# Optimization experiments

Measured on AMD Instinct MI355X. Metric: run time of the kernel, lower is better.

## Reference

```python
import jax, jax.numpy as jnp
import numpy as np

# ---- DMP constants (DMPParameters(N=5, tau=1, dt=1/(T*l), Dof=1)) ----
N = 5
T = 10
L_SUB = 10
DT = 1.0 / (T * L_SUB)          # 0.01
A_X = 1.0
A_Z = 25.0
B_Z = A_Z / 4.0
TIME_STEPS = T * L_SUB + 1       # 101
_C = jnp.exp(-A_X * jnp.linspace(0.0, 1.0, N)).astype(jnp.float32)        # RBF centers
_SIGMA2 = ((N ** 1.5) / _C / A_X).astype(jnp.float32)                     # RBF widths


def _conv1d(x, w, b, pad):
    # x: [B, Cin, L], w: [Cout, Cin, K]
    y = jax.lax.conv_general_dilated(x, w, window_strides=(1,), padding=[(pad, pad)],
                                     dimension_numbers=("NCH", "OIH", "NCH"))
    return y + b[None, :, None]


def _forward(input, y0, conv1_w, conv1_b, conv2_w, conv2_b, fc_w, fc_b, L_w, L_b):
    B = input.shape[0]
    # ---- TSFEEGNet (CNN feature extractor) -> [B, 404] ----
    h = jax.nn.relu(_conv1d(input, conv1_w, conv1_b, 3))     # [B, 64, 384]
    h = h.reshape(B, h.shape[1], -1, 4).mean(-1)             # avgpool4 -> [B, 64, 96]
    h = jax.nn.relu(_conv1d(h, conv2_w, conv2_b, 2))         # [B, 128, 96]
    h = h.reshape(B, h.shape[1], -1, 4).mean(-1)             # [B, 128, 24]
    feat = h.reshape(B, -1)                                  # [B, 3072]
    output = feat @ fc_w.T + fc_b                            # [B, 404]
    # ---- s = L(output): per-sample time scaling tau ----
    s = output @ L_w.T + L_b                                 # [B, 1]
    tau = s[:, 0]                                            # [B]
    # ---- DMPIntegrator.forward (Dof=1): goal=output[:,0], w=output[:,1:6] ----
    goal = output[:, 0]                                      # [B]
    w = output[:, 1:1 + N]                                   # [B, N]
    y0v = y0.reshape(-1)                                     # [B]
    dy0 = jnp.zeros_like(y0v) + 0.01

    def step(carry, _):
        x, y, z = carry
        x = x + (-A_X * x * tau * DT)                        # canonical system
        psi = jnp.exp(-0.5 * (x[:, None] - _C[None, :]) ** 2 / _SIGMA2[None, :])  # [B, N]
        fx = (w * psi).sum(-1) * x * (goal - y0v) / psi.sum(-1)
        dz = A_Z * (B_Z * (goal - y) - z) + fx
        dy = z
        y = y + dy * tau * DT
        z = z + dz * tau * DT
        return (x, y, z), y

    x0 = jnp.ones_like(y0v)
    z0 = dy0 * tau
    _, Ys = jax.lax.scan(step, (x0, y0v, z0), None, length=TIME_STEPS - 1)  # [T-1, B]
    Y = jnp.concatenate([y0v[None, :], Ys], axis=0)          # [T, B]
    y_traj = Y.T.reshape(B, 1, TIME_STEPS)                   # [B, Dof=1, T]
    return y_traj.transpose(0, 2, 1)                         # [B, T, 1]


def setup_inputs():
    key = jax.random.key(0)
    ks = jax.random.split(key, 10)
    B = 4096
    sc = 0.05
    return {
        "input": jax.random.normal(ks[0], (B, 5, 384), jnp.float32),
        "y0": jax.random.normal(ks[1], (B,), jnp.float32),
        "conv1_w": jax.random.normal(ks[2], (64, 5, 7), jnp.float32) * sc,
        "conv1_b": jax.random.normal(ks[3], (64,), jnp.float32) * sc,
        "conv2_w": jax.random.normal(ks[4], (128, 64, 5), jnp.float32) * sc,
        "conv2_b": jax.random.normal(ks[5], (128,), jnp.float32) * sc,
        "fc_w": jax.random.normal(ks[6], (404, 3072), jnp.float32) * sc,
        "fc_b": jax.random.normal(ks[7], (404,), jnp.float32) * sc,
        "L_w": jax.random.normal(ks[8], (1, 404), jnp.float32) * sc,
        "L_b": jax.random.normal(ks[9], (1,), jnp.float32) * sc,
    }


def reference(input, y0, conv1_w, conv1_b, conv2_w, conv2_b, fc_w, fc_b, L_w, L_b):
    return _forward(input, y0, conv1_w, conv1_b, conv2_w, conv2_b, fc_w, fc_b, L_w, L_b)
```

## Files before the change

kernel.cpp:

```cpp
#include <hip/hip_runtime.h>
#include <math.h>


typedef short bf16x8 __attribute__((ext_vector_type(8)));
typedef _Float16 f16x8 __attribute__((ext_vector_type(8)));
typedef float f32x4  __attribute__((ext_vector_type(4)));
typedef float f32x16 __attribute__((ext_vector_type(16)));
typedef int   i32x4  __attribute__((ext_vector_type(4)));

union Frag { int u[4]; i32x4 q; bf16x8 v; f16x8 h; };
union H16 { _Float16 hf; unsigned short us; };

__device__ __forceinline__ unsigned short f16_rne(float f) {
    H16 c; c.hf = (_Float16)f; return c.us;
}

#define ZERO16 {0.f,0.f,0.f,0.f,0.f,0.f,0.f,0.f,0.f,0.f,0.f,0.f,0.f,0.f,0.f,0.f}

__global__ void precompute_kernel(const float* __restrict__ w1,
                                  const float* __restrict__ w2,
                                  const float* __restrict__ fc_w,
                                  const float* __restrict__ fc_b,
                                  const float* __restrict__ L_w,
                                  const float* __restrict__ L_b,
                                  float* __restrict__ fc7,
                                  float* __restrict__ taub,
                                  unsigned* __restrict__ wfrag1,
                                  unsigned* __restrict__ wfrag2) {
    const int t = threadIdx.x, bb = blockIdx.x;
    if (bb < 48) {
        __shared__ float part[7][64];
        const int k = bb * 64 + (t & 63), jc = t >> 6;
        const int j0 = jc * 51;
        float s = 0.f;
        #pragma unroll 8
        for (int j = j0; j < j0 + 51 && j < 404; ++j)
            s += L_w[j] * fc_w[j * 3072 + k];
        if (jc) part[jc - 1][t & 63] = s;
        __syncthreads();
        if (jc == 0) {
            const int kk = t & 63;
            const int oc = k / 24, fq = k - oc * 24;
            float r[8];
            #pragma unroll
            for (int j = 0; j < 6; ++j) r[j] = fc_w[j * 3072 + k];
            float tv = s;
            #pragma unroll
            for (int j = 0; j < 7; ++j) tv += part[j][kk];
            r[6] = tv; r[7] = 0.f;
            #pragma unroll
            for (int j = 0; j < 8; ++j) fc7[fq * 1024 + j * 128 + oc] = r[j];
        }
    } else if (bb == 48) {
        if (t < 64) {
            float s = 0.f;
            for (int j = t; j < 404; j += 64) s += L_w[j] * fc_b[j];
            #pragma unroll
            for (int off = 32; off; off >>= 1) s += __shfl_down(s, off);
            if (t == 0) taub[0] = s + L_b[0];
        }
        for (int i = t; i < 768; i += 512) {
            const int part = i & 1, lane = (i >> 1) & 63,
                      nt = (i >> 7) & 1, ks = i >> 8;
            const int oc = nt * 32 + (lane & 31);
            unsigned short h[8];
            #pragma unroll
            for (int j = 0; j < 8; ++j) {
                const int kp = ks * 16 + (lane >> 5) * 8 + j;
                const int ic = kp >> 3, dk = kp & 7;
                const float v = (ic < 5 && dk < 7)
                              ? w1[oc * 35 + ic * 7 + dk] * 1024.0f : 0.f;
                H16 c; c.hf = (_Float16)v;
                if (part) { const float rr = v - (float)c.hf; c.hf = (_Float16)rr; }
                h[j] = c.us;
            }
            #pragma unroll
            for (int wj = 0; wj < 4; ++wj)
                wfrag1[i * 4 + wj] = ((unsigned)h[2 * wj + 1] << 16) | h[2 * wj];
        }
    } else {
        const int i = (bb - 49) * 512 + t;
        const int lane = i & 63, nt = (i >> 6) & 3, step = i >> 8;
        const int oc = nt * 32 + (lane & 31);
        const int dk = step >> 2, icc = step & 3;
        unsigned short h[8];
        #pragma unroll
        for (int j = 0; j < 8; ++j) {
            const int ic = icc * 16 + (lane >> 5) * 8 + j;
            const float v = w2[oc * 320 + ic * 5 + dk] * 1024.0f;
            h[j] = f16_rne(v);
        }
        #pragma unroll
        for (int wj = 0; wj < 4; ++wj)
            wfrag2[i * 4 + wj] = ((unsigned)h[2 * wj + 1] << 16) | h[2 * wj];
    }
}

__global__ __launch_bounds__(256, 4) void fused_kernel(
    const float* __restrict__ input,
    const float* __restrict__ b1,
    const float* __restrict__ b2,
    const unsigned* __restrict__ wfrag1,
    const unsigned* __restrict__ wfrag2,
    const float* __restrict__ fc7,
    const float* __restrict__ fc_b,
    const float* __restrict__ taubp,
    float* __restrict__ params)
{
    __shared__ unsigned lds_in[1960];
    __shared__ __align__(16) unsigned short h1f[7200];
    __shared__ float red[32];

    const int t = threadIdx.x, b = blockIdx.x;
    const int lane = t & 63, w = t >> 6;
    const int lq = lane & 31, hi = lane >> 5;

    for (int i = t; i < 1960; i += 256) lds_in[i] = 0u;
    if (t < 144) {
        const int r = t / 36, wd = t - r * 36;
        const int row = (r < 2) ? r : 96 + r;
        ((unsigned*)h1f)[row * 36 + wd] = 0u;
    }
    __syncthreads();
    const float* inb = input + (size_t)b * 1920;
    for (int i = t; i < 1920; i += 256) {
        const int ic = i / 384, x = i - ic * 384;
        lds_in[ic * 392 + 3 + x] = (unsigned)f16_rne(inb[i]);
    }
    __syncthreads();

    const i32x4* w1f = (const i32x4*)wfrag1;
    Frag c1b[3][2][2];
    #pragma unroll
    for (int ks = 0; ks < 3; ++ks)
        #pragma unroll
        for (int nt = 0; nt < 2; ++nt) {
            const int fi = ((ks * 2 + nt) * 64 + lane) * 2;
            c1b[ks][nt][0].q = w1f[fi];
            c1b[ks][nt][1].q = w1f[fi + 1];
        }
    float b1v[2];
    #pragma unroll
    for (int nt = 0; nt < 2; ++nt) b1v[nt] = b1[nt * 32 + lq];

    unsigned pbuf[2][8];
    {
        const unsigned* src = lds_in + hi * 392 + (w * 3) * 32 + lq;
        #pragma unroll
        for (int j = 0; j < 8; ++j) pbuf[0][j] = src[j];
    }
    #pragma unroll
    for (int m = 0; m < 3; ++m) {
        const int mtile = w * 3 + m;
        f32x16 acc0 = ZERO16, acc1 = ZERO16;
        #pragma unroll
        for (int ks = 0; ks < 3; ++ks) {
            const int it = m * 3 + ks, cur = it & 1, nxt = cur ^ 1;
            if (it < 8) {
                const int nit = it + 1, nm = nit / 3, nks = nit % 3;
                const int rowoff = (nks == 2) ? 4 * 392 : (nks * 2 + hi) * 392;
                const unsigned* src = lds_in + rowoff + (w * 3 + nm) * 32 + lq;
                #pragma unroll
                for (int j = 0; j < 8; ++j) pbuf[nxt][j] = src[j];
            }
            Frag af;
            #pragma unroll
            for (int wj = 0; wj < 4; ++wj)
                af.u[wj] = __builtin_amdgcn_perm(pbuf[cur][2*wj+1], pbuf[cur][2*wj], 0x05040100u);
            if (ks == 2) {
                #pragma unroll
                for (int wj = 0; wj < 4; ++wj) af.u[wj] = hi ? 0 : af.u[wj];
            }
            __builtin_amdgcn_s_setprio(1);
            acc0 = __builtin_amdgcn_mfma_f32_32x32x16_f16(af.h, c1b[ks][0][0].h, acc0, 0, 0, 0);
            acc1 = __builtin_amdgcn_mfma_f32_32x32x16_f16(af.h, c1b[ks][1][0].h, acc1, 0, 0, 0);
            acc0 = __builtin_amdgcn_mfma_f32_32x32x16_f16(af.h, c1b[ks][0][1].h, acc0, 0, 0, 0);
            acc1 = __builtin_amdgcn_mfma_f32_32x32x16_f16(af.h, c1b[ks][1][1].h, acc1, 0, 0, 0);
            __builtin_amdgcn_s_setprio(0);
        }
        #pragma unroll
        for (int q = 0; q < 4; ++q) {
            const int c = mtile * 8 + 2 * q + hi;
            {
                float s = 0.f;
                #pragma unroll
                for (int r4 = 0; r4 < 4; ++r4)
                    s += fmaxf(acc0[q*4+r4] * 0.0009765625f + b1v[0], 0.f);
                h1f[(c + 2) * 72 + lq] = f16_rne(0.25f * s);
            }
            {
                float s = 0.f;
                #pragma unroll
                for (int r4 = 0; r4 < 4; ++r4)
                    s += fmaxf(acc1[q*4+r4] * 0.0009765625f + b1v[1], 0.f);
                h1f[(c + 2) * 72 + 32 + lq] = f16_rne(0.25f * s);
            }
        }
    }
    __syncthreads();

    f32x16 acc2[3] = {ZERO16, ZERO16, ZERO16};

    const i32x4* aF = (const i32x4*)(h1f + lq * 72 + hi * 8);
    const i32x4* w2f = (const i32x4*)wfrag2;
    Frag b2b[2];
    Frag a2f[2][3];

    {
        b2b[0].q = w2f[w * 64 + lane];
        #pragma unroll
        for (int mt = 0; mt < 3; ++mt) a2f[0][mt].q = aF[mt * 288];
    }

    #pragma unroll
    for (int s = 0; s < 20; ++s) {
        const int sb = s & 1, nb = sb ^ 1;
        if (s < 19) {
            b2b[nb].q = w2f[((s + 1) * 4 + w) * 64 + lane];
            const int dkn = (s + 1) >> 2, iccn = (s + 1) & 3;
            #pragma unroll
            for (int mt = 0; mt < 3; ++mt)
                a2f[nb][mt].q = aF[(mt * 32 + dkn) * 9 + iccn * 2];
        }
        __builtin_amdgcn_s_setprio(1);
        #pragma unroll
        for (int mt = 0; mt < 3; ++mt)
            acc2[mt] = __builtin_amdgcn_mfma_f32_32x32x16_f16(a2f[sb][mt].h, b2b[sb].h, acc2[mt], 0, 0, 0);
        __builtin_amdgcn_s_setprio(0);
    }

    float dot[7] = {0.f, 0.f, 0.f, 0.f, 0.f, 0.f, 0.f};
    {
        const float b2v = b2[w * 32 + lq];
        #pragma unroll
        for (int mt = 0; mt < 3; ++mt) {
            #pragma unroll
            for (int q = 0; q < 4; ++q) {
                float s = 0.f;
                #pragma unroll
                for (int r4 = 0; r4 < 4; ++r4)
                    s += fmaxf(acc2[mt][q*4+r4] * 0.0009765625f + b2v, 0.f);
                s *= 0.25f;
                const int fq = mt * 8 + 2 * q + hi;
                const float* fp = fc7 + fq * 1024 + w * 32 + lq;
                float f[7];
                #pragma unroll
                for (int j = 0; j < 7; ++j) f[j] = fp[j * 128];
                #pragma unroll
                for (int j = 0; j < 7; ++j) dot[j] += s * f[j];
            }
        }
    }

    #pragma unroll
    for (int j = 0; j < 7; ++j) {
        float s = dot[j];
        #pragma unroll
        for (int off = 32; off; off >>= 1) s += __shfl_down(s, off);
        if (lane == 0) red[w * 8 + j] = s;
    }
    __syncthreads();
    if (t < 7) {
        float s = red[t] + red[8 + t] + red[16 + t] + red[24 + t];
        s += (t < 6) ? fc_b[t] : taubp[0];
        params[(size_t)b * 8 + t] = s;
    }
}

__global__ void rollout_kernel(const float* __restrict__ params,
                               const float* __restrict__ y0,
                               float* __restrict__ out) {
    const int b = blockIdx.x * 256 + threadIdx.x;
    const float* p = params + (size_t)b * 8;
    const float goal = p[0];
    const float w0 = p[1], w1 = p[2], w2 = p[3], w3 = p[4], w4 = p[5];
    const float tau = p[6];
    const float y0v = y0[b];

    const float c0 = 1.0f;
    const float c1 = 0.77880078307140486825f;
    const float c2 = 0.60653065971263342360f;
    const float c3 = 0.47236655274101470714f;
    const float c4 = 0.36787944117144232160f;
    const float inv2s = -0.5f / 11.180339887498949f;
    const float e0 = inv2s * c0, e1 = inv2s * c1, e2 = inv2s * c2,
                e3 = inv2s * c3, e4 = inv2s * c4;

    float x = 1.0f, y = y0v, z = 0.01f * tau;
    const float td = tau * 0.01f;
    const float gmy0 = goal - y0v;
    float* ob = out + (size_t)b * 101;
    ob[0] = y0v;
    for (int s = 1; s <= 100; ++s) {
        x = x - x * td;
        const float d0 = x - c0, d1 = x - c1, d2 = x - c2, d3 = x - c3, d4 = x - c4;
        const float p0 = __expf(e0 * d0 * d0);
        const float p1 = __expf(e1 * d1 * d1);
        const float p2 = __expf(e2 * d2 * d2);
        const float p3 = __expf(e3 * d3 * d3);
        const float p4 = __expf(e4 * d4 * d4);
        const float den = p0 + p1 + p2 + p3 + p4;
        const float num = w0 * p0 + w1 * p1 + w2 * p2 + w3 * p3 + w4 * p4;
        const float fx = (num / den) * x * gmy0;
        const float dz = 25.0f * (6.25f * (goal - y) - z) + fx;
        const float dy = z;
        y += dy * td;
        z += dz * td;
        ob[s] = y;
    }
}

extern "C" void kernel_launch(void* const* d_in, const int* in_sizes, int n_in,
                              void* d_out, int out_size, void* d_ws, size_t ws_size,
                              hipStream_t stream) {
    const float* input = (const float*)d_in[0];
    const float* y0    = (const float*)d_in[1];
    const float* w1    = (const float*)d_in[2];
    const float* b1    = (const float*)d_in[3];
    const float* w2    = (const float*)d_in[4];
    const float* b2    = (const float*)d_in[5];
    const float* fc_w  = (const float*)d_in[6];
    const float* fc_b  = (const float*)d_in[7];
    const float* L_w   = (const float*)d_in[8];
    const float* L_b   = (const float*)d_in[9];
    float* out = (float*)d_out;

    float* ws      = (float*)d_ws;
    float* fc7     = ws;
    float* taub    = ws + 24576;
    float* params  = ws + 24640;
    unsigned* wfrag1 = (unsigned*)(ws + 57408);
    unsigned* wfrag2 = wfrag1 + 4096;

    const int B = in_sizes[1];

    precompute_kernel<<<59, 512, 0, stream>>>(w1, w2, fc_w, fc_b, L_w, L_b,
                                              fc7, taub, wfrag1, wfrag2);
    fused_kernel<<<B, 256, 0, stream>>>(input, b1, b2, wfrag1, wfrag2,
                                        fc7, fc_b, taub, params);
    rollout_kernel<<<B / 256, 256, 0, stream>>>(params, y0, out);
}
```

Before: 92.53 us.

## Split fused conv kernel work across 12 waves per block instead of 4

Raises the fused kernel's block size from 256 to 768 threads so that each of 12 waves computes a single 32x32 output tile for conv1 and for conv2, instead of 4 waves each doing 3 tiles with software-pipelined prefetch. The aim is more wave-level parallelism to hide MFMA and LDS latency, with fewer registers needed per wave. The cost is losing the register-level prefetch pipelining, more waves contending for the same LDS, a 12-way final reduction, and a launch-bound change that affects how many blocks fit per CU.

```diff
diff --git a/kernel.cpp b/kernel.cpp
--- a/kernel.cpp
+++ b/kernel.cpp
@@ -2,13 +2,11 @@
 #include <math.h>
 
 
-typedef short bf16x8 __attribute__((ext_vector_type(8)));
 typedef _Float16 f16x8 __attribute__((ext_vector_type(8)));
-typedef float f32x4  __attribute__((ext_vector_type(4)));
 typedef float f32x16 __attribute__((ext_vector_type(16)));
 typedef int   i32x4  __attribute__((ext_vector_type(4)));
 
-union Frag { int u[4]; i32x4 q; bf16x8 v; f16x8 h; };
+union Frag { int u[4]; i32x4 q; f16x8 h; };
 union H16 { _Float16 hf; unsigned short us; };
 
 __device__ __forceinline__ unsigned short f16_rne(float f) {
@@ -96,7 +94,7 @@
     }
 }
 
-__global__ __launch_bounds__(256, 4) void fused_kernel(
+__global__ __launch_bounds__(768, 6) void fused_kernel(
     const float* __restrict__ input,
     const float* __restrict__ b1,
     const float* __restrict__ b2,
@@ -109,13 +107,13 @@
 {
     __shared__ unsigned lds_in[1960];
     __shared__ __align__(16) unsigned short h1f[7200];
-    __shared__ float red[32];
+    __shared__ float red[96];
 
     const int t = threadIdx.x, b = blockIdx.x;
     const int lane = t & 63, w = t >> 6;
     const int lq = lane & 31, hi = lane >> 5;
 
-    for (int i = t; i < 1960; i += 256) lds_in[i] = 0u;
+    for (int i = t; i < 1960; i += 768) lds_in[i] = 0u;
     if (t < 144) {
         const int r = t / 36, wd = t - r * 36;
         const int row = (r < 2) ? r : 96 + r;
@@ -123,132 +121,93 @@
     }
     __syncthreads();
     const float* inb = input + (size_t)b * 1920;
-    for (int i = t; i < 1920; i += 256) {
+    for (int i = t; i < 1920; i += 768) {
         const int ic = i / 384, x = i - ic * 384;
         lds_in[ic * 392 + 3 + x] = (unsigned)f16_rne(inb[i]);
     }
     __syncthreads();
 
     const i32x4* w1f = (const i32x4*)wfrag1;
-    Frag c1b[3][2][2];
     #pragma unroll
-    for (int ks = 0; ks < 3; ++ks)
-        #pragma unroll
-        for (int nt = 0; nt < 2; ++nt) {
+    for (int nt = 0; nt < 2; ++nt) {
+        f32x16 acc = ZERO16;
+        #pragma unroll
+        for (int ks = 0; ks < 3; ++ks) {
             const int fi = ((ks * 2 + nt) * 64 + lane) * 2;
-            c1b[ks][nt][0].q = w1f[fi];
-            c1b[ks][nt][1].q = w1f[fi + 1];
-        }
-    float b1v[2];
-    #pragma unroll
-    for (int nt = 0; nt < 2; ++nt) b1v[nt] = b1[nt * 32 + lq];
-
-    unsigned pbuf[2][8];
-    {
-        const unsigned* src = lds_in + hi * 392 + (w * 3) * 32 + lq;
-        #pragma unroll
-        for (int j = 0; j < 8; ++j) pbuf[0][j] = src[j];
-    }
-    #pragma unroll
-    for (int m = 0; m < 3; ++m) {
-        const int mtile = w * 3 + m;
-        f32x16 acc0 = ZERO16, acc1 = ZERO16;
-        #pragma unroll
-        for (int ks = 0; ks < 3; ++ks) {
-            const int it = m * 3 + ks, cur = it & 1, nxt = cur ^ 1;
-            if (it < 8) {
-                const int nit = it + 1, nm = nit / 3, nks = nit % 3;
-                const int rowoff = (nks == 2) ? 4 * 392 : (nks * 2 + hi) * 392;
-                const unsigned* src = lds_in + rowoff + (w * 3 + nm) * 32 + lq;
-                #pragma unroll
-                for (int j = 0; j < 8; ++j) pbuf[nxt][j] = src[j];
-            }
+            Frag bh, bl;
+            bh.q = ((const i32x4*)wfrag1)[fi];
+            bl.q = ((const i32x4*)wfrag1)[fi + 1];
+            const int rowoff = (ks == 2) ? 4 * 392 : (ks * 2 + hi) * 392;
+            const unsigned* src = lds_in + rowoff + w * 32 + lq;
+            unsigned p[8];
+            #pragma unroll
+            for (int j = 0; j < 8; ++j) p[j] = src[j];
             Frag af;
             #pragma unroll
             for (int wj = 0; wj < 4; ++wj)
-                af.u[wj] = __builtin_amdgcn_perm(pbuf[cur][2*wj+1], pbuf[cur][2*wj], 0x05040100u);
+                af.u[wj] = __builtin_amdgcn_perm(p[2*wj+1], p[2*wj], 0x05040100u);
             if (ks == 2) {
                 #pragma unroll
                 for (int wj = 0; wj < 4; ++wj) af.u[wj] = hi ? 0 : af.u[wj];
             }
             __builtin_amdgcn_s_setprio(1);
-            acc0 = __builtin_amdgcn_mfma_f32_32x32x16_f16(af.h, c1b[ks][0][0].h, acc0, 0, 0, 0);
-            acc1 = __builtin_amdgcn_mfma_f32_32x32x16_f16(af.h, c1b[ks][1][0].h, acc1, 0, 0, 0);
-            acc0 = __builtin_amdgcn_mfma_f32_32x32x16_f16(af.h, c1b[ks][0][1].h, acc0, 0, 0, 0);
-            acc1 = __builtin_amdgcn_mfma_f32_32x32x16_f16(af.h, c1b[ks][1][1].h, acc1, 0, 0, 0);
+            acc = __builtin_amdgcn_mfma_f32_32x32x16_f16(af.h, bh.h, acc, 0, 0, 0);
+            acc = __builtin_amdgcn_mfma_f32_32x32x16_f16(af.h, bl.h, acc, 0, 0, 0);
             __builtin_amdgcn_s_setprio(0);
         }
+        const float b1v = b1[nt * 32 + lq];
         #pragma unroll
         for (int q = 0; q < 4; ++q) {
-            const int c = mtile * 8 + 2 * q + hi;
-            {
-                float s = 0.f;
-                #pragma unroll
-                for (int r4 = 0; r4 < 4; ++r4)
-                    s += fmaxf(acc0[q*4+r4] * 0.0009765625f + b1v[0], 0.f);
-                h1f[(c + 2) * 72 + lq] = f16_rne(0.25f * s);
-            }
-            {
-                float s = 0.f;
-                #pragma unroll
-                for (int r4 = 0; r4 < 4; ++r4)
-                    s += fmaxf(acc1[q*4+r4] * 0.0009765625f + b1v[1], 0.f);
-                h1f[(c + 2) * 72 + 32 + lq] = f16_rne(0.25f * s);
-            }
+            const int c = w * 8 + 2 * q + hi;
+            float s = 0.f;
+            #pragma unroll
+            for (int r4 = 0; r4 < 4; ++r4)
+                s += fmaxf(acc[q*4+r4] * 0.0009765625f + b1v, 0.f);
+            h1f[(c + 2) * 72 + nt * 32 + lq] = f16_rne(0.25f * s);
         }
     }
     __syncthreads();
 
-    f32x16 acc2[3] = {ZERO16, ZERO16, ZERO16};
+    const int nt2 = w & 3, mt = w >> 2;
+    f32x16 acc2 = ZERO16;
 
     const i32x4* aF = (const i32x4*)(h1f + lq * 72 + hi * 8);
     const i32x4* w2f = (const i32x4*)wfrag2;
-    Frag b2b[2];
-    Frag a2f[2][3];
-
-    {
-        b2b[0].q = w2f[w * 64 + lane];
-        #pragma unroll
-        for (int mt = 0; mt < 3; ++mt) a2f[0][mt].q = aF[mt * 288];
-    }
+    Frag b2b[2], a2f[2];
+
+    b2b[0].q = w2f[nt2 * 64 + lane];
+    a2f[0].q = aF[mt * 288];
 
     #pragma unroll
     for (int s = 0; s < 20; ++s) {
         const int sb = s & 1, nb = sb ^ 1;
         if (s < 19) {
-            b2b[nb].q = w2f[((s + 1) * 4 + w) * 64 + lane];
+            b2b[nb].q = w2f[((s + 1) * 4 + nt2) * 64 + lane];
             const int dkn = (s + 1) >> 2, iccn = (s + 1) & 3;
-            #pragma unroll
-            for (int mt = 0; mt < 3; ++mt)
-                a2f[nb][mt].q = aF[(mt * 32 + dkn) * 9 + iccn * 2];
+            a2f[nb].q = aF[(mt * 32 + dkn) * 9 + iccn * 2];
         }
         __builtin_amdgcn_s_setprio(1);
-        #pragma unroll
-        for (int mt = 0; mt < 3; ++mt)
-            acc2[mt] = __builtin_amdgcn_mfma_f32_32x32x16_f16(a2f[sb][mt].h, b2b[sb].h, acc2[mt], 0, 0, 0);
+        acc2 = __builtin_amdgcn_mfma_f32_32x32x16_f16(a2f[sb].h, b2b[sb].h, acc2, 0, 0, 0);
         __builtin_amdgcn_s_setprio(0);
     }
 
     float dot[7] = {0.f, 0.f, 0.f, 0.f, 0.f, 0.f, 0.f};
     {
-        const float b2v = b2[w * 32 + lq];
-        #pragma unroll
-        for (int mt = 0; mt < 3; ++mt) {
-            #pragma unroll
-            for (int q = 0; q < 4; ++q) {
-                float s = 0.f;
-                #pragma unroll
-                for (int r4 = 0; r4 < 4; ++r4)
-                    s += fmaxf(acc2[mt][q*4+r4] * 0.0009765625f + b2v, 0.f);
-                s *= 0.25f;
-                const int fq = mt * 8 + 2 * q + hi;
-                const float* fp = fc7 + fq * 1024 + w * 32 + lq;
-                float f[7];
-                #pragma unroll
-                for (int j = 0; j < 7; ++j) f[j] = fp[j * 128];
-                #pragma unroll
-                for (int j = 0; j < 7; ++j) dot[j] += s * f[j];
-            }
+        const float b2v = b2[nt2 * 32 + lq];
+        #pragma unroll
+        for (int q = 0; q < 4; ++q) {
+            float s = 0.f;
+            #pragma unroll
+            for (int r4 = 0; r4 < 4; ++r4)
+                s += fmaxf(acc2[q*4+r4] * 0.0009765625f + b2v, 0.f);
+            s *= 0.25f;
+            const int fq = mt * 8 + 2 * q + hi;
+            const float* fp = fc7 + fq * 1024 + nt2 * 32 + lq;
+            float f[7];
+            #pragma unroll
+            for (int j = 0; j < 7; ++j) f[j] = fp[j * 128];
+            #pragma unroll
+            for (int j = 0; j < 7; ++j) dot[j] += s * f[j];
         }
     }
 
@@ -261,8 +220,9 @@
     }
     __syncthreads();
     if (t < 7) {
-        float s = red[t] + red[8 + t] + red[16 + t] + red[24 + t];
-        s += (t < 6) ? fc_b[t] : taubp[0];
+        float s = (t < 6) ? fc_b[t] : taubp[0];
+        #pragma unroll
+        for (int k = 0; k < 12; ++k) s += red[k * 8 + t];
         params[(size_t)b * 8 + t] = s;
     }
 }
@@ -336,7 +296,7 @@
 
     precompute_kernel<<<59, 512, 0, stream>>>(w1, w2, fc_w, fc_b, L_w, L_b,
                                               fc7, taub, wfrag1, wfrag2);
-    fused_kernel<<<B, 256, 0, stream>>>(input, b1, b2, wfrag1, wfrag2,
+    fused_kernel<<<B, 768, 0, stream>>>(input, b1, b2, wfrag1, wfrag2,
                                         fc7, fc_b, taub, params);
     rollout_kernel<<<B / 256, 256, 0, stream>>>(params, y0, out);
 }
```

Result: slower. 114.5 us (+23.7%).
